# Performance work log

Measured on AMD Instinct MI355X. Metric: run time of the kernel, lower is better.

The kernel has to match this reference:

```python
import jax, jax.numpy as jnp
import numpy as np

S, T, F, J, E, H = 1024, 64, 128, 64, 256, 4
DH = E // H


def layer_norm(x, g, b, eps=1e-10):
    m = jnp.mean(x, axis=-1, keepdims=True)
    v = jnp.mean((x - m) ** 2, axis=-1, keepdims=True)  # population var (correction=0)
    return (x - m) / jnp.sqrt(v + eps) * g + b


def mha(x, Wq, Wk, Wv):
    # x: [B, L, E]; Wq/Wk/Wv: [H, E, DH]. Non-standard: scale AFTER softmax@V.
    q = jnp.einsum('ble,hed->hbld', x, Wq)
    k = jnp.einsum('ble,hed->hbld', x, Wk)
    v = jnp.einsum('ble,hed->hbld', x, Wv)
    w = jax.nn.softmax(jnp.einsum('hbld,hbmd->hblm', q, k), axis=-1)
    o = jnp.einsum('hblm,hbmd->hbld', w, v) / jnp.sqrt(jnp.asarray(Wq.shape[-1], x.dtype))
    h, b, l, d = o.shape
    return jnp.transpose(o, (1, 2, 0, 3)).reshape(b, l, h * d)


def ffn(x, W1, b1, W2, b2):
    return jnp.maximum(x @ W1 + b1, 0.0) @ W2 + b2  # Dropout is identity in eval


def pos_encoding(t, e):
    pos = jnp.arange(t, dtype=jnp.float32)[:, None]
    two_i = jnp.floor(jnp.arange(e, dtype=jnp.float32) / 2.0) * 2.0
    div = jnp.power(jnp.float32(100004.0), two_i / e)
    pe = pos / div  # [t, e]
    pe = pe.at[:, 0::2].set(jnp.sin(pe[:, 0::2]))
    pe = pe.at[:, 1::2].set(jnp.cos(pe[:, 1::2]))
    return pe


def setup_inputs() -> dict:
    key = jax.random.key(0)
    ks = jax.random.split(key, 32)
    s = 0.02
    d = {}
    d['x'] = jax.random.normal(ks[0], (S, T, F + J), dtype=jnp.float32)
    d['gate_W'] = s * jax.random.normal(ks[1], (J, F))
    d['gate_b'] = s * jax.random.normal(ks[2], (F,))
    d['embed_W'] = s * jax.random.normal(ks[3], (F, E))
    d['ln0_g'] = 1.0 + s * jax.random.normal(ks[4], (E,))
    d['ln0_b'] = s * jax.random.normal(ks[5], (E,))
    d['intra_Wq'] = s * jax.random.normal(ks[6], (H, E, DH))
    d['intra_Wk'] = s * jax.random.normal(ks[7], (H, E, DH))
    d['intra_Wv'] = s * jax.random.normal(ks[8], (H, E, DH))
    d['intra_ln_g'] = 1.0 + s * jax.random.normal(ks[9], (E,))
    d['intra_ln_b'] = s * jax.random.normal(ks[10], (E,))
    d['intra_W1'] = s * jax.random.normal(ks[11], (E, 4 * E))
    d['intra_b1'] = s * jax.random.normal(ks[12], (4 * E,))
    d['intra_W2'] = s * jax.random.normal(ks[13], (4 * E, E))
    d['intra_b2'] = s * jax.random.normal(ks[14], (E,))
    d['inter_Wq'] = s * jax.random.normal(ks[15], (H, E, DH))
    d['inter_Wk'] = s * jax.random.normal(ks[16], (H, E, DH))
    d['inter_Wv'] = s * jax.random.normal(ks[17], (H, E, DH))
    d['inter_ln1_g'] = 1.0 + s * jax.random.normal(ks[18], (E,))
    d['inter_ln1_b'] = s * jax.random.normal(ks[19], (E,))
    d['inter_ln2_g'] = 1.0 + s * jax.random.normal(ks[20], (E,))
    d['inter_ln2_b'] = s * jax.random.normal(ks[21], (E,))
    d['inter_W1'] = s * jax.random.normal(ks[22], (E, 4 * E))
    d['inter_b1'] = s * jax.random.normal(ks[23], (4 * E,))
    d['inter_W2'] = s * jax.random.normal(ks[24], (4 * E, E))
    d['inter_b2'] = s * jax.random.normal(ks[25], (E,))
    d['temp_W'] = s * jax.random.normal(ks[26], (E, E))
    d['pred_W'] = s * jax.random.normal(ks[27], (E, 1))
    d['pred_b'] = s * jax.random.normal(ks[28], (1,))
    return d


def reference(x, gate_W, gate_b, embed_W, ln0_g, ln0_b,
              intra_Wq, intra_Wk, intra_Wv, intra_ln_g, intra_ln_b,
              intra_W1, intra_b1, intra_W2, intra_b2,
              inter_Wq, inter_Wk, inter_Wv, inter_ln1_g, inter_ln1_b,
              inter_ln2_g, inter_ln2_b, inter_W1, inter_b1, inter_W2, inter_b2,
              temp_W, pred_W, pred_b):
    # Gating
    x_f = x[..., :F]                       # [S, T, F]
    x_g = x[..., -1, F:]                   # [S, J]
    gate = jax.nn.softmax(x_g @ gate_W + gate_b, axis=-1)[:, None, :]
    x_f = gate * x_f
    # Embed + positional encoding + LN
    emb = x_f @ embed_W                    # [S, T, E]
    res = emb + pos_encoding(T, E)
    ln = layer_norm(res, ln0_g, ln0_b)
    # Intra-stock attention (attend over time axis per stock)
    a = mha(ln, intra_Wq, intra_Wk, intra_Wv)
    r = a + ln
    intra_out = r + ffn(layer_norm(r, intra_ln_g, intra_ln_b), intra_W1, intra_b1, intra_W2, intra_b2)
    # Inter-stock attention (attend over stock axis per timestep)
    xT = jnp.transpose(intra_out, (1, 0, 2))            # [T, S, E]
    xTn = layer_norm(xT, inter_ln1_g, inter_ln1_b)
    a2 = mha(xTn, inter_Wq, inter_Wk, inter_Wv)          # [T, S, E]
    out = jnp.transpose(a2, (1, 0, 2))                   # [S, T, E]
    r2 = out + intra_out
    inter_out = r2 + ffn(layer_norm(r2, inter_ln2_g, inter_ln2_b), inter_W1, inter_b1, inter_W2, inter_b2)
    # Temporal aggregation
    x1 = inter_out @ temp_W                              # [S, T, E]
    cur = x1[..., -1, :][..., :, None]                   # [S, E, 1]
    lam = jax.nn.softmax(jnp.squeeze(x1 @ cur, -1), axis=-1)[:, None, :]  # [S, 1, T]
    agg = jnp.squeeze(lam @ inter_out, -2)               # [S, E]
    # Prediction
    return agg @ pred_W + pred_b                         # [S, 1]
```

## Files before the change

kernel.cpp:

```cpp
#include <hip/hip_runtime.h>


typedef _Float16 h16;
typedef __attribute__((ext_vector_type(8))) _Float16 f16x8;
typedef __attribute__((ext_vector_type(4))) _Float16 f16x4;
typedef __attribute__((ext_vector_type(4))) float f32x4;

__device__ inline float wave_sum(float v){
  #pragma unroll
  for (int o=32;o;o>>=1) v += __shfl_xor(v,o);
  return v;
}
__device__ inline float wave_max(float v){
  #pragma unroll
  for (int o=32;o;o>>=1) v = fmaxf(v,__shfl_xor(v,o));
  return v;
}

__global__ __launch_bounds__(256) void k_pe(float* __restrict__ pe){
  int t = blockIdx.x, i = threadIdx.x;
  float two_i = (float)((i>>1)<<1);
  float dv = powf(100004.0f, two_i*(1.0f/256.0f));
  float v = (float)t / dv;
  pe[t*256+i] = (i&1) ? cosf(v) : sinf(v);
}

__global__ __launch_bounds__(64) void k_gate(const float* __restrict__ x,
    const float* __restrict__ gW, const float* __restrict__ gb,
    float* __restrict__ gate){
  int s = blockIdx.x, lane = threadIdx.x;
  __shared__ float xg[64];
  xg[lane] = x[((size_t)s*64+63)*192 + 128 + lane];
  __syncthreads();
  float a0 = gb[lane], a1 = gb[64+lane];
  #pragma unroll 4
  for (int j=0;j<64;j++){
    float xv = xg[j];
    a0 += xv*gW[j*128+lane];
    a1 += xv*gW[j*128+64+lane];
  }
  float mx = wave_max(fmaxf(a0,a1));
  float e0 = __expf(a0-mx), e1 = __expf(a1-mx);
  float sm = wave_sum(e0+e1);
  gate[s*128+lane]    = e0/sm;
  gate[s*128+64+lane] = e1/sm;
}

__global__ __launch_bounds__(256) void k_t16all(
    const float* __restrict__ q1, const float* __restrict__ k1, const float* __restrict__ v1,
    const float* __restrict__ q2, const float* __restrict__ k2, const float* __restrict__ v2,
    const float* __restrict__ embed_W, const float* __restrict__ temp_W,
    const float* __restrict__ iW1, const float* __restrict__ iW2,
    const float* __restrict__ eW1, const float* __restrict__ eW2,
    h16* __restrict__ base){
  __shared__ float tile[32][33];
  const int b = blockIdx.x, tid = threadIdx.x;
  const float* src; h16* dst; int K, N, tb; bool qkv = false;
  if (b < 384){
    int mat = b>>6; tb = b&63; qkv = true; K = 256; N = 256;
    src = (mat==0)?q1:(mat==1)?k1:(mat==2)?v1:(mat==3)?q2:(mat==4)?k2:v2;
    dst = base + mat*65536;
  } else if (b < 416){ tb = b-384;  K=128;  N=256;  src=embed_W; dst=base+393216; }
  else if (b < 480){ tb = b-416;  K=256;  N=256;  src=temp_W;  dst=base+425984; }
  else if (b < 736){ tb = b-480;  K=256;  N=1024; src=iW1;     dst=base+491520; }
  else if (b < 992){ tb = b-736;  K=1024; N=256;  src=iW2;     dst=base+753664; }
  else if (b < 1248){ tb = b-992; K=256;  N=1024; src=eW1;     dst=base+1015808; }
  else               { tb = b-1248; K=1024; N=256; src=eW2;    dst=base+1277952; }
  const int nt = N>>5;
  const int N0 = (tb & (nt-1))<<5;
  const int K0 = (tb/nt)<<5;
  {
    int r = tid>>3, c0 = (tid&7)<<2;
    int k = K0+r, n = N0+c0;
    const float* p = qkv ? (src + ((n>>6)<<14) + (k<<6) + (n&63))
                         : (src + (size_t)k*N + n);
    float4 v = *(const float4*)p;
    tile[r][c0]=v.x; tile[r][c0+1]=v.y; tile[r][c0+2]=v.z; tile[r][c0+3]=v.w;
  }
  __syncthreads();
  {
    int r = tid>>3, c0 = (tid&7)<<2;
    f16x4 o;
    o[0]=(h16)tile[c0][r]; o[1]=(h16)tile[c0+1][r];
    o[2]=(h16)tile[c0+2][r]; o[3]=(h16)tile[c0+3][r];
    *(f16x4*)(dst + (size_t)(N0+r)*K + K0 + c0) = o;
  }
}

__global__ __launch_bounds__(256) void k_embed(
    const float* __restrict__ x, const h16* __restrict__ Et,
    const float* __restrict__ pe, const float* __restrict__ gate,
    const float* __restrict__ g0, const float* __restrict__ b0,
    float* __restrict__ A){
  __shared__ char pool[65536];
  h16*  As  = (h16*)pool;
  float* res = (float*)pool;
  const int tid = threadIdx.x, lane = tid&63, w = tid>>6;
  const int lr = lane&15, g = lane>>4;
  const int m0 = blockIdx.x<<6;
  #pragma unroll
  for (int it=0; it<8; it++){
    int f4 = it*256 + tid;
    int row = f4>>5, c4 = (f4&31)<<2;
    float4 v = *(const float4*)(x + (size_t)(m0+row)*192 + c4);
    float4 gg = *(const float4*)(gate + (((m0+row)>>6)<<7) + c4);
    v.x*=gg.x; v.y*=gg.y; v.z*=gg.z; v.w*=gg.w;
    int idx = ((row<<7) + c4) ^ ((row&7)<<3);
    f16x4 o; o[0]=(h16)v.x; o[1]=(h16)v.y; o[2]=(h16)v.z; o[3]=(h16)v.w;
    *(f16x4*)&As[idx] = o;
  }
  __syncthreads();
  f32x4 acc[4][4];
  #pragma unroll
  for (int a=0;a<4;a++)
    #pragma unroll
    for (int b=0;b<4;b++) acc[a][b] = (f32x4){0,0,0,0};
  #pragma unroll
  for (int i=0; i<4; i++){
    int kt = (i + w) & 3;
    f16x8 af[4], bf[4];
    #pragma unroll
    for (int rf=0; rf<4; rf++){
      int r = (rf<<4) + lr;
      int idx = ((r<<7) + (kt<<5) + (g<<3)) ^ ((r&7)<<3);
      af[rf] = *(const f16x8*)&As[idx];
    }
    #pragma unroll
    for (int cf=0; cf<4; cf++){
      int n = (w<<6) + (cf<<4) + lr;
      bf[cf] = *(const f16x8*)(Et + (size_t)n*128 + (kt<<5) + (g<<3));
    }
    __builtin_amdgcn_s_setprio(1);
    #pragma unroll
    for (int rf=0; rf<4; rf++)
      #pragma unroll
      for (int cf=0; cf<4; cf++)
        acc[rf][cf] = __builtin_amdgcn_mfma_f32_16x16x32_f16(af[rf], bf[cf], acc[rf][cf], 0,0,0);
    __builtin_amdgcn_s_setprio(0);
  }
  __syncthreads();
  #pragma unroll
  for (int cf=0; cf<4; cf++){
    int col = (w<<6) + (cf<<4) + lr;
    #pragma unroll
    for (int rf=0; rf<4; rf++)
      #pragma unroll
      for (int i=0;i<4;i++){
        int r = (rf<<4) + (g<<2) + i;
        res[(r<<8) + col] = acc[rf][cf][i] + pe[(r<<8) + col];
      }
  }
  __syncthreads();
  {
    float4 gg = *(const float4*)(g0 + (lane<<2));
    float4 bb = *(const float4*)(b0 + (lane<<2));
    for (int rr=0; rr<16; rr++){
      int r = (w<<4) + rr;
      float4 v = *(float4*)&res[(r<<8) + (lane<<2)];
      float sm = wave_sum(v.x+v.y+v.z+v.w);
      float sq = wave_sum(v.x*v.x+v.y*v.y+v.z*v.z+v.w*v.w);
      float mean = sm*(1.f/256.f);
      float rs = rsqrtf(sq*(1.f/256.f) - mean*mean + 1e-10f);
      float4 o;
      o.x=(v.x-mean)*rs*gg.x+bb.x; o.y=(v.y-mean)*rs*gg.y+bb.y;
      o.z=(v.z-mean)*rs*gg.z+bb.z; o.w=(v.w-mean)*rs*gg.w+bb.w;
      *(float4*)(A + (size_t)(m0+r)*256 + (lane<<2)) = o;
    }
  }
}

__global__ __launch_bounds__(512,1) void k_intra(
    const float* __restrict__ A, const h16* __restrict__ Wqkv,
    float* __restrict__ Out){
  __shared__ h16 Xs[64*256];
  __shared__ h16 Qs[4*64*64];
  __shared__ h16 Ks[4*64*64];
  __shared__ h16 VsT[4*64*64];
  __shared__ h16 Ps[8*16*64];
  const int tid = threadIdx.x, lane = tid&63, w = tid>>6;
  const int lr = lane&15, g = lane>>4;
  const int m0 = blockIdx.x<<6;

  #pragma unroll
  for (int rr=0; rr<8; rr++){
    int r = (w<<3) + rr;
    float4 v = *(const float4*)(A + (size_t)(m0+r)*256 + (lane<<2));
    f16x4 o; o[0]=(h16)v.x; o[1]=(h16)v.y; o[2]=(h16)v.z; o[3]=(h16)v.w;
    int idx = ((r<<8) + (lane<<2)) ^ ((r&7)<<3);
    *(f16x4*)&Xs[idx] = o;
  }
  __syncthreads();

  f32x4 acc[4][6];
  #pragma unroll
  for (int a=0;a<4;a++)
    #pragma unroll
    for (int b=0;b<6;b++) acc[a][b] = (f32x4){0,0,0,0};
  #pragma unroll
  for (int kt=0; kt<8; kt++){
    f16x8 af[4], bf[6];
    #pragma unroll
    for (int rf=0; rf<4; rf++){
      int r = (rf<<4) + lr;
      int idx = ((r<<8) + (kt<<5) + (g<<3)) ^ ((r&7)<<3);
      af[rf] = *(const f16x8*)&Xs[idx];
    }
    #pragma unroll
    for (int m=0;m<3;m++)
      #pragma unroll
      for (int cf=0;cf<2;cf++){
        int n = (w<<5) + (cf<<4) + lr;
        bf[m*2+cf] = *(const f16x8*)(Wqkv + (size_t)m*65536 + (size_t)n*256 + (kt<<5) + (g<<3));
      }
    __builtin_amdgcn_s_setprio(1);
    #pragma unroll
    for (int rf=0; rf<4; rf++)
      #pragma unroll
      for (int mc=0; mc<6; mc++)
        acc[rf][mc] = __builtin_amdgcn_mfma_f32_16x16x32_f16(af[rf], bf[mc], acc[rf][mc], 0,0,0);
    __builtin_amdgcn_s_setprio(0);
  }
  #pragma unroll
  for (int cf=0; cf<2; cf++){
    int n = (w<<5) + (cf<<4) + lr;
    int head = n>>6, d = n&63;
    int hb = head<<12;
    int vkey = (d + (d>>3)) & 7;
    #pragma unroll
    for (int rf=0; rf<4; rf++)
      #pragma unroll
      for (int i=0;i<4;i++){
        int qrow = (rf<<4) + (g<<2) + i;
        Qs[hb + (qrow<<6) + (((d>>3) ^ (qrow&7))<<3) + (d&7)] = (h16)acc[rf][0*2+cf][i];
        Ks[hb + (qrow<<6) + (((d>>3) ^ (qrow&7))<<3) + (d&7)] = (h16)acc[rf][1*2+cf][i];
        VsT[hb + (d<<6) + (((qrow>>3) ^ vkey)<<3) + (qrow&7)] = (h16)acc[rf][2*2+cf][i];
      }
  }
  __syncthreads();

  #pragma unroll
  for (int sl=0; sl<2; sl++){
    int slot = w + (sl<<3);
    int head = slot>>2, q0 = (slot&3)<<4;
    const int hb = head<<12;
    f16x8 qf[2];
    #pragma unroll
    for (int ks=0; ks<2; ks++)
      qf[ks] = *(const f16x8*)&Qs[hb + ((q0+lr)<<6) + (((g + (ks<<2)) ^ (lr&7))<<3)];
    f32x4 sa[4];
    #pragma unroll
    for (int mm=0;mm<4;mm++) sa[mm] = (f32x4){0,0,0,0};
    __builtin_amdgcn_s_setprio(1);
    #pragma unroll
    for (int ks=0; ks<2; ks++)
      #pragma unroll
      for (int mm=0;mm<4;mm++){
        int krow = (mm<<4) + lr;
        f16x8 af = *(const f16x8*)&Ks[hb + (krow<<6) + (((g + (ks<<2)) ^ (krow&7))<<3)];
        sa[mm] = __builtin_amdgcn_mfma_f32_16x16x32_f16(af, qf[ks], sa[mm], 0,0,0);
      }
    __builtin_amdgcn_s_setprio(0);
    float pmax = -1e30f;
    #pragma unroll
    for (int mm=0;mm<4;mm++)
      #pragma unroll
      for (int i=0;i<4;i++) pmax = fmaxf(pmax, sa[mm][i]);
    pmax = fmaxf(pmax, __shfl_xor(pmax, 16));
    pmax = fmaxf(pmax, __shfl_xor(pmax, 32));
    float ps = 0.f;
    f16x4 pv[4];
    #pragma unroll
    for (int mm=0;mm<4;mm++)
      #pragma unroll
      for (int i=0;i<4;i++){
        float p = __expf(sa[mm][i] - pmax);
        ps += p;
        pv[mm][i] = (h16)p;
      }
    ps += __shfl_xor(ps, 16);
    ps += __shfl_xor(ps, 32);
    const int pbase = w<<10;
    #pragma unroll
    for (int mm=0;mm<4;mm++){
      int k0 = (mm<<4) + (g<<2);
      int unit = k0>>3, off = k0&7;
      *(f16x4*)&Ps[pbase + (lr<<6) + ((unit ^ (lr&7))<<3) + off] = pv[mm];
    }
    f32x4 oc[4];
    #pragma unroll
    for (int cf=0;cf<4;cf++) oc[cf] = (f32x4){0,0,0,0};
    __builtin_amdgcn_s_setprio(1);
    #pragma unroll
    for (int ks=0; ks<2; ks++){
      f16x8 pa = *(const f16x8*)&Ps[pbase + (lr<<6) + (((g + (ks<<2)) ^ (lr&7))<<3)];
      #pragma unroll
      for (int cf=0;cf<4;cf++){
        int d = (cf<<4) + lr;
        int key = (d + (d>>3)) & 7;
        f16x8 bf = *(const f16x8*)&VsT[hb + (d<<6) + (((g + (ks<<2)) ^ key)<<3)];
        oc[cf] = __builtin_amdgcn_mfma_f32_16x16x32_f16(pa, bf, oc[cf], 0,0,0);
      }
    }
    __builtin_amdgcn_s_setprio(0);
    float linv = 1.0f/(ps*8.0f);
    #pragma unroll
    for (int i=0;i<4;i++){
      float li = __shfl(linv, (g<<4) + (g<<2) + i);
      int row = m0 + q0 + (g<<2) + i;
      #pragma unroll
      for (int cf=0;cf<4;cf++){
        int col = (head<<6) + (cf<<4) + lr;
        size_t ga = (size_t)row*256 + col;
        Out[ga] = oc[cf][i]*li + A[ga];
      }
    }
  }
}

template<bool DOLN>
__global__ __launch_bounds__(512) void k_qkv(
    const float* __restrict__ X,
    const float* __restrict__ lng, const float* __restrict__ lnb,
    const h16* __restrict__ Bt0,
    h16* __restrict__ Qh, h16* __restrict__ Kh, h16* __restrict__ Vh){
  __shared__ h16 Xs[64*256];
  const int tid = threadIdx.x, lane = tid&63, w = tid>>6;
  const int lr = lane&15, g = lane>>4;
  const int m0 = blockIdx.x<<6;
  {
    float4 gg, bb;
    if (DOLN){ gg = *(const float4*)(lng + (lane<<2)); bb = *(const float4*)(lnb + (lane<<2)); }
    #pragma unroll
    for (int rr=0; rr<8; rr++){
      int r = (w<<3) + rr;
      float4 v = *(const float4*)(X + (size_t)(m0+r)*256 + (lane<<2));
      if (DOLN){
        float sm = wave_sum(v.x+v.y+v.z+v.w);
        float sq = wave_sum(v.x*v.x+v.y*v.y+v.z*v.z+v.w*v.w);
        float mean = sm*(1.f/256.f);
        float rs = rsqrtf(sq*(1.f/256.f) - mean*mean + 1e-10f);
        v.x=(v.x-mean)*rs*gg.x+bb.x; v.y=(v.y-mean)*rs*gg.y+bb.y;
        v.z=(v.z-mean)*rs*gg.z+bb.z; v.w=(v.w-mean)*rs*gg.w+bb.w;
      }
      f16x4 o; o[0]=(h16)v.x; o[1]=(h16)v.y; o[2]=(h16)v.z; o[3]=(h16)v.w;
      int idx = ((r<<8) + (lane<<2)) ^ ((r&7)<<3);
      *(f16x4*)&Xs[idx] = o;
    }
  }
  __syncthreads();
  f32x4 acc[4][3];
  #pragma unroll
  for (int a=0;a<4;a++)
    #pragma unroll
    for (int m=0;m<3;m++) acc[a][m] = (f32x4){0,0,0,0};
  #pragma unroll
  for (int i=0; i<8; i++){
    int kt = (i + w) & 7;
    f16x8 af[4], bf[3];
    #pragma unroll
    for (int rf=0; rf<4; rf++){
      int r = (rf<<4) + lr;
      int idx = ((r<<8) + (kt<<5) + (g<<3)) ^ ((r&7)<<3);
      af[rf] = *(const f16x8*)&Xs[idx];
    }
    #pragma unroll
    for (int m=0;m<3;m++){
      int n = (w<<4) + lr;
      bf[m] = *(const f16x8*)(Bt0 + (size_t)m*65536 + (size_t)n*256 + (kt<<5) + (g<<3));
    }
    __builtin_amdgcn_s_setprio(1);
    #pragma unroll
    for (int rf=0; rf<4; rf++)
      #pragma unroll
      for (int m=0;m<3;m++)
        acc[rf][m] = __builtin_amdgcn_mfma_f32_16x16x32_f16(af[rf], bf[m], acc[rf][m], 0,0,0);
    __builtin_amdgcn_s_setprio(0);
  }
  const int col = (w<<4) + lr;
  #pragma unroll
  for (int m=0;m<3;m++){
    h16* dst = (m==0)?Qh:(m==1)?Kh:Vh;
    #pragma unroll
    for (int rf=0; rf<4; rf++)
      #pragma unroll
      for (int i=0;i<4;i++){
        int r = m0 + (rf<<4) + (g<<2) + i;
        dst[(size_t)r*128 + col] = (h16)acc[rf][m][i];
      }
  }
}

template<int NT, int QG>
__global__ __launch_bounds__(256) void k_attn16(
    const h16* __restrict__ Qh, const h16* __restrict__ Kh, const h16* __restrict__ Vh,
    const float* __restrict__ Resid, float* __restrict__ Out, int hbase){
  __shared__ h16 Ks[64*64];
  __shared__ h16 VsT[64*64];
  __shared__ h16 Ps[4*QG*16*64];
  const int tid = threadIdx.x, lane = tid&63, w = tid>>6;
  const int lr = lane&15, g = lane>>4;
  int hh, t=0, qc=0, s=0;
  if (NT==1){ s = blockIdx.x; hh = blockIdx.y; }
  else      { hh = blockIdx.x; t = blockIdx.y; qc = blockIdx.z; }
  const int ccol = hh<<6;
  const int gcol = (hbase+hh)<<6;

  f16x8 qf[QG][2];
  #pragma unroll
  for (int grp=0; grp<QG; grp++){
    int ql = grp*64 + (w<<4) + lr;
    size_t m = (NT==1) ? ((size_t)s*64 + ql) : (((size_t)qc*(64*QG) + ql)*64 + t);
    const h16* qp = Qh + m*128 + ccol + (g<<3);
    qf[grp][0] = *(const f16x8*)qp;
    qf[grp][1] = *(const f16x8*)(qp + 32);
  }

  f32x4 oc[QG][4];
  float m_r[QG], l_r[QG];
  #pragma unroll
  for (int grp=0; grp<QG; grp++){
    #pragma unroll
    for (int cf=0;cf<4;cf++) oc[grp][cf] = (f32x4){0,0,0,0};
    m_r[grp] = -1e30f; l_r[grp] = 0.f;
  }

  for (int kb=0; kb<NT; kb++){
    __syncthreads();
    #pragma unroll
    for (int it=0; it<2; it++){
      int u = it*256 + tid;
      int row = u>>3, un = u&7;
      size_t m = (NT==1) ? ((size_t)s*64 + row) : (((size_t)kb*64 + row)*64 + t);
      f16x8 kv = *(const f16x8*)(Kh + m*128 + ccol + (un<<3));
      *(f16x8*)&Ks[(row<<6) + ((un ^ (row&7))<<3)] = kv;
      f16x8 vv = *(const f16x8*)(Vh + m*128 + ccol + (un<<3));
      #pragma unroll
      for (int j=0;j<8;j++){
        int d = (un<<3) + j;
        int key = (d + un) & 7;
        VsT[(d<<6) + ((((row>>3) ^ key))<<3) + (row&7)] = vv[j];
      }
    }
    __syncthreads();
    #pragma unroll
    for (int grp=0; grp<QG; grp++){
      f32x4 sa[4];
      #pragma unroll
      for (int mm=0;mm<4;mm++) sa[mm] = (f32x4){0,0,0,0};
      __builtin_amdgcn_s_setprio(1);
      #pragma unroll
      for (int ks=0; ks<2; ks++){
        #pragma unroll
        for (int mm=0;mm<4;mm++){
          int krow = (mm<<4) + lr;
          f16x8 af = *(const f16x8*)&Ks[(krow<<6) + (((g + (ks<<2)) ^ (krow&7))<<3)];
          sa[mm] = __builtin_amdgcn_mfma_f32_16x16x32_f16(af, qf[grp][ks], sa[mm], 0,0,0);
        }
      }
      __builtin_amdgcn_s_setprio(0);
      float pmax = -1e30f;
      #pragma unroll
      for (int mm=0;mm<4;mm++)
        #pragma unroll
        for (int i=0;i<4;i++) pmax = fmaxf(pmax, sa[mm][i]);
      pmax = fmaxf(pmax, __shfl_xor(pmax, 16));
      pmax = fmaxf(pmax, __shfl_xor(pmax, 32));
      float mn = fmaxf(m_r[grp], pmax);
      float sca = __expf(m_r[grp] - mn);
      m_r[grp] = mn;
      float ps = 0.f;
      f16x4 pv[4];
      #pragma unroll
      for (int mm=0;mm<4;mm++){
        #pragma unroll
        for (int i=0;i<4;i++){
          float p = __expf(sa[mm][i] - mn);
          ps += p;
          pv[mm][i] = (h16)p;
        }
      }
      ps += __shfl_xor(ps, 16);
      ps += __shfl_xor(ps, 32);
      l_r[grp] = l_r[grp]*sca + ps;
      const int pbase = ((w*QG + grp)<<10);
      #pragma unroll
      for (int mm=0;mm<4;mm++){
        int k0 = (mm<<4) + (g<<2);
        int unit = k0>>3, off = k0&7;
        *(f16x4*)&Ps[pbase + (lr<<6) + ((unit ^ (lr&7))<<3) + off] = pv[mm];
      }
      #pragma unroll
      for (int i=0;i<4;i++){
        float si = __shfl(sca, (g<<4) + (g<<2) + i);
        #pragma unroll
        for (int cf=0;cf<4;cf++) oc[grp][cf][i] *= si;
      }
      __builtin_amdgcn_s_setprio(1);
      #pragma unroll
      for (int ks=0; ks<2; ks++){
        f16x8 pa = *(const f16x8*)&Ps[pbase + (lr<<6) + (((g + (ks<<2)) ^ (lr&7))<<3)];
        #pragma unroll
        for (int cf=0;cf<4;cf++){
          int d = (cf<<4) + lr;
          int key = (d + (d>>3)) & 7;
          f16x8 bf = *(const f16x8*)&VsT[(d<<6) + (((g + (ks<<2)) ^ key)<<3)];
          oc[grp][cf] = __builtin_amdgcn_mfma_f32_16x16x32_f16(pa, bf, oc[grp][cf], 0,0,0);
        }
      }
      __builtin_amdgcn_s_setprio(0);
    }
  }
  #pragma unroll
  for (int grp=0; grp<QG; grp++){
    float linv = 1.0f/(l_r[grp]*8.0f);
    #pragma unroll
    for (int i=0;i<4;i++){
      float li = __shfl(linv, (g<<4) + (g<<2) + i);
      int ql = grp*64 + (w<<4) + (g<<2) + i;
      size_t m = (NT==1) ? ((size_t)s*64 + ql) : (((size_t)qc*(64*QG) + ql)*64 + t);
      #pragma unroll
      for (int cf=0;cf<4;cf++){
        int d = (cf<<4) + lr;
        size_t ga = m*256 + gcol + d;
        Out[ga] = oc[grp][cf][i]*li + Resid[ga];
      }
    }
  }
}

__global__ __launch_bounds__(512,1) void k_ffn5(
    const float* X, float* Out,
    const float* __restrict__ lng, const float* __restrict__ lnb,
    const h16* __restrict__ W1t, const float* __restrict__ b1,
    const h16* __restrict__ W2t, const float* __restrict__ b2){
  __shared__ h16 Xs[64*256];
  __shared__ h16 Hc[64*1024];
  const int tid  = threadIdx.x;
  const int lane = tid & 63;
  const int w    = tid >> 6;
  const int r0   = blockIdx.x << 6;
  const int lr   = lane & 15;
  const int g    = lane >> 4;
  {
    float4 gg = *(const float4*)(lng + (lane<<2));
    float4 bb = *(const float4*)(lnb + (lane<<2));
    #pragma unroll
    for (int rr=0; rr<8; rr++){
      int r = (w<<3) + rr;
      float4 v = *(const float4*)(X + (size_t)(r0+r)*256 + (lane<<2));
      float sm = wave_sum(v.x+v.y+v.z+v.w);
      float sq = wave_sum(v.x*v.x+v.y*v.y+v.z*v.z+v.w*v.w);
      float mean = sm*(1.f/256.f);
      float rs = rsqrtf(sq*(1.f/256.f) - mean*mean + 1e-10f);
      f16x4 o;
      o[0]=(h16)((v.x-mean)*rs*gg.x+bb.x); o[1]=(h16)((v.y-mean)*rs*gg.y+bb.y);
      o[2]=(h16)((v.z-mean)*rs*gg.z+bb.z); o[3]=(h16)((v.w-mean)*rs*gg.w+bb.w);
      int idx = ((r<<8) + (lane<<2)) ^ ((r&7)<<3);
      *(f16x4*)&Xs[idx] = o;
    }
  }
  __syncthreads();
  {
    f32x4 acc1[4][8];
    #pragma unroll
    for (int a=0;a<4;a++)
      #pragma unroll
      for (int b=0;b<8;b++) acc1[a][b] = (f32x4){0,0,0,0};
    #pragma unroll
    for (int i=0; i<8; i++){
      int kt = (i + w) & 7;
      f16x8 af[4], bf[8];
      #pragma unroll
      for (int rf=0; rf<4; rf++){
        int r = (rf<<4) + lr;
        int idx = ((r<<8) + (kt<<5) + (g<<3)) ^ ((r&7)<<3);
        af[rf] = *(const f16x8*)&Xs[idx];
      }
      #pragma unroll
      for (int cf=0; cf<8; cf++){
        int n = (w<<7) + (cf<<4) + lr;
        bf[cf] = *(const f16x8*)(W1t + (size_t)n*256 + (kt<<5) + (g<<3));
      }
      __builtin_amdgcn_s_setprio(1);
      #pragma unroll
      for (int rf=0; rf<4; rf++)
        #pragma unroll
        for (int cf=0; cf<8; cf++)
          acc1[rf][cf] = __builtin_amdgcn_mfma_f32_16x16x32_f16(
              af[rf], bf[cf], acc1[rf][cf], 0, 0, 0);
      __builtin_amdgcn_s_setprio(0);
    }
    #pragma unroll
    for (int cf=0; cf<8; cf++){
      int cl = (w<<7) + (cf<<4) + lr;
      float bv = b1[cl];
      #pragma unroll
      for (int rf=0; rf<4; rf++){
        #pragma unroll
        for (int i=0;i<4;i++){
          int r = (rf<<4) + (g<<2) + i;
          float hv = fmaxf(acc1[rf][cf][i] + bv, 0.f);
          int idx = ((r<<10) + cl) ^ ((r&7)<<3);
          Hc[idx] = (h16)hv;
        }
      }
    }
  }
  __syncthreads();
  f32x4 acc2[4][2];
  #pragma unroll
  for (int a=0;a<4;a++){ acc2[a][0]=(f32x4){0,0,0,0}; acc2[a][1]=(f32x4){0,0,0,0}; }
  #pragma unroll 4
  for (int i=0; i<32; i++){
    int kt = (i + (w<<2)) & 31;
    f16x8 af[4], bf[2];
    #pragma unroll
    for (int rf=0; rf<4; rf++){
      int r = (rf<<4) + lr;
      int idx = ((r<<10) + (kt<<5) + (g<<3)) ^ ((r&7)<<3);
      af[rf] = *(const f16x8*)&Hc[idx];
    }
    #pragma unroll
    for (int cf=0; cf<2; cf++){
      int n = (w<<5) + (cf<<4) + lr;
      bf[cf] = *(const f16x8*)(W2t + (size_t)n*1024 + (kt<<5) + (g<<3));
    }
    __builtin_amdgcn_s_setprio(1);
    #pragma unroll
    for (int rf=0; rf<4; rf++)
      #pragma unroll
      for (int cf=0; cf<2; cf++)
        acc2[rf][cf] = __builtin_amdgcn_mfma_f32_16x16x32_f16(
            af[rf], bf[cf], acc2[rf][cf], 0, 0, 0);
    __builtin_amdgcn_s_setprio(0);
  }
  #pragma unroll
  for (int cf=0; cf<2; cf++){
    int col = (w<<5) + (cf<<4) + lr;
    float bv = b2[col];
    #pragma unroll
    for (int rf=0; rf<4; rf++){
      #pragma unroll
      for (int i=0;i<4;i++){
        size_t r = (size_t)r0 + (rf<<4) + (g<<2) + i;
        float res = X[r*256 + col];
        Out[r*256 + col] = acc2[rf][cf][i] + bv + res;
      }
    }
  }
}

__global__ __launch_bounds__(256) void k_head(
    const float* __restrict__ Bb, const h16* __restrict__ Tt,
    const float* __restrict__ predW, const float* __restrict__ predb,
    float* __restrict__ out){
  __shared__ h16 Xs[64*256];
  __shared__ float X1s[64*256];
  __shared__ float lam[64];
  __shared__ float red[4];
  const int tid = threadIdx.x, lane = tid&63, w = tid>>6;
  const int lr = lane&15, g = lane>>4;
  const size_t m0 = (size_t)blockIdx.x<<6;
  #pragma unroll
  for (int it=0; it<16; it++){
    int f4 = it*256 + tid;
    int row = f4>>6, c4 = (f4&63)<<2;
    float4 v = *(const float4*)(Bb + (m0+row)*256 + c4);
    int idx = ((row<<8) + c4) ^ ((row&7)<<3);
    f16x4 o; o[0]=(h16)v.x; o[1]=(h16)v.y; o[2]=(h16)v.z; o[3]=(h16)v.w;
    *(f16x4*)&Xs[idx] = o;
  }
  __syncthreads();
  f32x4 acc[4][4];
  #pragma unroll
  for (int rf=0;rf<4;rf++)
    #pragma unroll
    for (int cf=0;cf<4;cf++) acc[rf][cf] = (f32x4){0,0,0,0};
  #pragma unroll
  for (int kt=0; kt<8; kt++){
    f16x8 af[4], bf[4];
    #pragma unroll
    for (int rf=0; rf<4; rf++){
      int r = (rf<<4) + lr;
      int idx = ((r<<8) + (kt<<5) + (g<<3)) ^ ((r&7)<<3);
      af[rf] = *(const f16x8*)&Xs[idx];
    }
    #pragma unroll
    for (int cf=0; cf<4; cf++){
      int n = (w<<6) + (cf<<4) + lr;
      bf[cf] = *(const f16x8*)(Tt + (size_t)n*256 + (kt<<5) + (g<<3));
    }
    __builtin_amdgcn_s_setprio(1);
    #pragma unroll
    for (int rf=0; rf<4; rf++)
      #pragma unroll
      for (int cf=0; cf<4; cf++)
        acc[rf][cf] = __builtin_amdgcn_mfma_f32_16x16x32_f16(af[rf], bf[cf], acc[rf][cf], 0,0,0);
    __builtin_amdgcn_s_setprio(0);
  }
  #pragma unroll
  for (int cf=0; cf<4; cf++){
    int col = (w<<6) + (cf<<4) + lr;
    #pragma unroll
    for (int rf=0; rf<4; rf++)
      #pragma unroll
      for (int i=0;i<4;i++){
        int r = (rf<<4) + (g<<2) + i;
        X1s[(r<<8) + col] = acc[rf][cf][i];
      }
  }
  __syncthreads();
  float lg[16];
  for (int r=0;r<16;r++){
    int trow = (w<<4) + r;
    float4 xa = *(float4*)&X1s[(trow<<8) + (lane<<2)];
    float4 xc = *(float4*)&X1s[(63<<8) + (lane<<2)];
    lg[r] = wave_sum(xa.x*xc.x + xa.y*xc.y + xa.z*xc.z + xa.w*xc.w);
  }
  if (lane==0){
    #pragma unroll
    for (int r=0;r<16;r++) lam[(w<<4)+r] = lg[r];
  }
  __syncthreads();
  if (tid < 64){
    float v = lam[tid];
    float mx = wave_max(v);
    float p = __expf(v-mx);
    float sm = wave_sum(p);
    lam[tid] = p/sm;
  }
  __syncthreads();
  float ag = 0.f;
  for (int t=0;t<64;t++)
    ag += lam[t]*(float)Xs[((t<<8)+tid) ^ ((t&7)<<3)];
  float wsum = wave_sum(ag * predW[tid]);
  if (lane==0) red[w] = wsum;
  __syncthreads();
  if (tid==0) out[blockIdx.x] = red[0]+red[1]+red[2]+red[3] + predb[0];
}

extern "C" void kernel_launch(void* const* d_in, const int* in_sizes, int n_in,
                              void* d_out, int out_size, void* d_ws, size_t ws_size,
                              hipStream_t stream){
  const float* x       = (const float*)d_in[0];
  const float* gate_W  = (const float*)d_in[1];
  const float* gate_b  = (const float*)d_in[2];
  const float* embed_W = (const float*)d_in[3];
  const float* ln0_g   = (const float*)d_in[4];
  const float* ln0_b   = (const float*)d_in[5];
  const float* iln_g   = (const float*)d_in[9];
  const float* iln_b   = (const float*)d_in[10];
  const float* iW1     = (const float*)d_in[11];
  const float* ib1     = (const float*)d_in[12];
  const float* iW2     = (const float*)d_in[13];
  const float* ib2     = (const float*)d_in[14];
  const float* eln1_g  = (const float*)d_in[18];
  const float* eln1_b  = (const float*)d_in[19];
  const float* eln2_g  = (const float*)d_in[20];
  const float* eln2_b  = (const float*)d_in[21];
  const float* eW1     = (const float*)d_in[22];
  const float* eb1     = (const float*)d_in[23];
  const float* eW2     = (const float*)d_in[24];
  const float* eb2     = (const float*)d_in[25];
  const float* temp_W  = (const float*)d_in[26];
  const float* pred_W  = (const float*)d_in[27];
  const float* pred_b  = (const float*)d_in[28];
  float* out = (float*)d_out;

  float* pe    = (float*)d_ws;
  float* gate  = pe + 16384;
  h16* fQKV = (h16*)((char*)d_ws + ((size_t)4<<20));
  h16* fE   = fQKV + 393216;
  h16* fT   = fE + 32768;
  h16* fW1i = fT + 65536;
  h16* fW2i = fW1i + 262144;
  h16* fW1e = fW2i + 262144;
  h16* fW2e = fW1e + 262144;
  const size_t MR = (size_t)65536*256, MH = (size_t)65536*128;
  float* A  = (float*)((char*)d_ws + ((size_t)8<<20));
  float* Bb = A + MR;
  h16* Qh = (h16*)(Bb + MR);
  h16* Kh = Qh + MH;
  h16* Vh = Kh + MH;

  k_pe  <<<64,  256, 0, stream>>>(pe);
  k_gate<<<1024, 64, 0, stream>>>(x, gate_W, gate_b, gate);
  k_t16all<<<1504,256,0,stream>>>(
      (const float*)d_in[6],(const float*)d_in[7],(const float*)d_in[8],
      (const float*)d_in[15],(const float*)d_in[16],(const float*)d_in[17],
      embed_W, temp_W, iW1, iW2, eW1, eW2, fQKV);

  k_embed<<<1024,256,0,stream>>>(x, fE, pe, gate, ln0_g, ln0_b, A);

  k_intra<<<1024,512,0,stream>>>(A, fQKV, Bb);
  k_ffn5<<<1024,512,0,stream>>>(Bb, Bb, iln_g, iln_b, fW1i, ib1, fW2i, ib2);

  for (int hp=0; hp<2; hp++){
    int hb = hp*2;
    k_qkv<true><<<1024,512,0,stream>>>(Bb, eln1_g, eln1_b,
        fQKV + 3*65536 + hb*16384, Qh, Kh, Vh);
    k_attn16<16,1><<<dim3(2,64,16),256,0,stream>>>(Qh, Kh, Vh, Bb, Bb, hb);
  }
  k_ffn5<<<1024,512,0,stream>>>(Bb, Bb, eln2_g, eln2_b, fW1e, eb1, fW2e, eb2);

  k_head<<<1024,256,0,stream>>>(Bb, fT, pred_W, pred_b, out);
}
```

Baseline: 722.9 us.

## Split FFN layernorm into separate kernel and restructure FFN with LDS-staged weight chunks

```diff
diff --git a/kernel.cpp b/kernel.cpp
--- a/kernel.cpp
+++ b/kernel.cpp
@@ -180,7 +180,6 @@
   const int tid = threadIdx.x, lane = tid&63, w = tid>>6;
   const int lr = lane&15, g = lane>>4;
   const int m0 = blockIdx.x<<6;
-
   #pragma unroll
   for (int rr=0; rr<8; rr++){
     int r = (w<<3) + rr;
@@ -190,7 +189,6 @@
     *(f16x4*)&Xs[idx] = o;
   }
   __syncthreads();
-
   f32x4 acc[4][6];
   #pragma unroll
   for (int a=0;a<4;a++)
@@ -237,7 +235,6 @@
       }
   }
   __syncthreads();
-
   #pragma unroll
   for (int sl=0; sl<2; sl++){
     int slot = w + (sl<<3);
@@ -528,126 +525,147 @@
   }
 }
 
-__global__ __launch_bounds__(512,1) void k_ffn5(
-    const float* X, float* Out,
-    const float* __restrict__ lng, const float* __restrict__ lnb,
+__global__ __launch_bounds__(256) void k_lnh(const float* __restrict__ in,
+    const float* __restrict__ g, const float* __restrict__ b,
+    h16* __restrict__ out){
+  const int wv = threadIdx.x>>6, lane = threadIdx.x&63;
+  const size_t row = (size_t)blockIdx.x*4 + wv;
+  float4 v = *(const float4*)(in + row*256 + (lane<<2));
+  float sm = wave_sum(v.x+v.y+v.z+v.w);
+  float sq = wave_sum(v.x*v.x+v.y*v.y+v.z*v.z+v.w*v.w);
+  float mean = sm*(1.f/256.f);
+  float rs = rsqrtf(sq*(1.f/256.f) - mean*mean + 1e-10f);
+  float4 gg = *(const float4*)(g + (lane<<2));
+  float4 bb = *(const float4*)(b + (lane<<2));
+  f16x4 o;
+  o[0]=(h16)((v.x-mean)*rs*gg.x+bb.x); o[1]=(h16)((v.y-mean)*rs*gg.y+bb.y);
+  o[2]=(h16)((v.z-mean)*rs*gg.z+bb.z); o[3]=(h16)((v.w-mean)*rs*gg.w+bb.w);
+  *(f16x4*)(out + row*256 + (lane<<2)) = o;
+}
+
+__global__ __launch_bounds__(512,1) void k_ffn7(
+    const h16* __restrict__ Xh, const float* __restrict__ Resid,
+    float* __restrict__ Out,
     const h16* __restrict__ W1t, const float* __restrict__ b1,
     const h16* __restrict__ W2t, const float* __restrict__ b2){
-  __shared__ h16 Xs[64*256];
-  __shared__ h16 Hc[64*1024];
-  const int tid  = threadIdx.x;
-  const int lane = tid & 63;
-  const int w    = tid >> 6;
-  const int r0   = blockIdx.x << 6;
-  const int lr   = lane & 15;
-  const int g    = lane >> 4;
-  {
-    float4 gg = *(const float4*)(lng + (lane<<2));
-    float4 bb = *(const float4*)(lnb + (lane<<2));
-    #pragma unroll
-    for (int rr=0; rr<8; rr++){
-      int r = (w<<3) + rr;
-      float4 v = *(const float4*)(X + (size_t)(r0+r)*256 + (lane<<2));
-      float sm = wave_sum(v.x+v.y+v.z+v.w);
-      float sq = wave_sum(v.x*v.x+v.y*v.y+v.z*v.z+v.w*v.w);
-      float mean = sm*(1.f/256.f);
-      float rs = rsqrtf(sq*(1.f/256.f) - mean*mean + 1e-10f);
-      f16x4 o;
-      o[0]=(h16)((v.x-mean)*rs*gg.x+bb.x); o[1]=(h16)((v.y-mean)*rs*gg.y+bb.y);
-      o[2]=(h16)((v.z-mean)*rs*gg.z+bb.z); o[3]=(h16)((v.w-mean)*rs*gg.w+bb.w);
-      int idx = ((r<<8) + (lane<<2)) ^ ((r&7)<<3);
-      *(f16x4*)&Xs[idx] = o;
-    }
-  }
-  __syncthreads();
-  {
-    f32x4 acc1[4][8];
-    #pragma unroll
-    for (int a=0;a<4;a++)
-      #pragma unroll
-      for (int b=0;b<8;b++) acc1[a][b] = (f32x4){0,0,0,0};
-    #pragma unroll
-    for (int i=0; i<8; i++){
-      int kt = (i + w) & 7;
-      f16x8 af[4], bf[8];
-      #pragma unroll
-      for (int rf=0; rf<4; rf++){
-        int r = (rf<<4) + lr;
-        int idx = ((r<<8) + (kt<<5) + (g<<3)) ^ ((r&7)<<3);
-        af[rf] = *(const f16x8*)&Xs[idx];
-      }
-      #pragma unroll
-      for (int cf=0; cf<8; cf++){
-        int n = (w<<7) + (cf<<4) + lr;
-        bf[cf] = *(const f16x8*)(W1t + (size_t)n*256 + (kt<<5) + (g<<3));
-      }
-      __builtin_amdgcn_s_setprio(1);
+  __shared__ h16 W1c[128*256];
+  __shared__ h16 W2c[256*128];
+  __shared__ h16 Pool[64*256];
+  const int tid = threadIdx.x, lane = tid&63, w = tid>>6;
+  const int lr = lane&15, g = lane>>4;
+  const size_t R0 = (size_t)blockIdx.x<<8;
+
+  float b2v[2];
+  b2v[0] = b2[(w<<5)+lr]; b2v[1] = b2[(w<<5)+16+lr];
+
+  f32x4 acc2[4][4][2];
+  #pragma unroll
+  for (int rt=0;rt<4;rt++)
+    #pragma unroll
+    for (int rf=0;rf<4;rf++){
+      acc2[rt][rf][0]=(f32x4){0,0,0,0}; acc2[rt][rf][1]=(f32x4){0,0,0,0};
+    }
+
+  for (int hc=0; hc<8; hc++){
+    __syncthreads();
+    {
+      int n1 = tid>>2, p1 = tid&3;
+      const h16* s1 = W1t + (size_t)((hc<<7) + n1)*256;
+      #pragma unroll
+      for (int j=0;j<8;j++){
+        int u = (p1<<3)+j;
+        *(f16x8*)&W1c[(n1<<8) + ((u ^ (n1&7))<<3)] = *(const f16x8*)(s1 + (u<<3));
+      }
+      int n2 = tid>>1, p2 = tid&1;
+      const h16* s2 = W2t + (size_t)n2*1024 + (hc<<7);
+      #pragma unroll
+      for (int j=0;j<8;j++){
+        int u = (p2<<3)+j;
+        *(f16x8*)&W2c[(n2<<7) + ((u ^ (n2&7))<<3)] = *(const f16x8*)(s2 + (u<<3));
+      }
+    }
+    float b1v = b1[(hc<<7) + (w<<4) + lr];
+
+    #pragma unroll
+    for (int rt=0; rt<4; rt++){
+      __syncthreads();
+      {
+        const h16* xsrc = Xh + (R0 + (rt<<6))*256;
+        #pragma unroll
+        for (int it=0; it<4; it++){
+          int e = it*512 + tid;
+          int row = e>>5, u = e&31;
+          *(f16x8*)&Pool[(row<<8) + ((u ^ (row&7))<<3)] =
+              *(const f16x8*)(xsrc + (row<<8) + (u<<3));
+        }
+      }
+      __syncthreads();
+      f32x4 acc1[4];
+      #pragma unroll
+      for (int rf=0;rf<4;rf++) acc1[rf] = (f32x4){0,0,0,0};
+      const int n1 = (w<<4) + lr;
+      #pragma unroll
+      for (int kt=0; kt<8; kt++){
+        f16x8 af[4];
+        #pragma unroll
+        for (int rf=0; rf<4; rf++){
+          int r = (rf<<4) + lr;
+          af[rf] = *(const f16x8*)&Pool[((r<<8) + (kt<<5) + (g<<3)) ^ ((r&7)<<3)];
+        }
+        f16x8 bf = *(const f16x8*)&W1c[(n1<<8) + ((((kt<<2)+g) ^ (n1&7))<<3)];
+        __builtin_amdgcn_s_setprio(1);
+        #pragma unroll
+        for (int rf=0; rf<4; rf++)
+          acc1[rf] = __builtin_amdgcn_mfma_f32_16x16x32_f16(af[rf], bf, acc1[rf], 0,0,0);
+        __builtin_amdgcn_s_setprio(0);
+      }
+      __syncthreads();
       #pragma unroll
       for (int rf=0; rf<4; rf++)
-        #pragma unroll
-        for (int cf=0; cf<8; cf++)
-          acc1[rf][cf] = __builtin_amdgcn_mfma_f32_16x16x32_f16(
-              af[rf], bf[cf], acc1[rf][cf], 0, 0, 0);
-      __builtin_amdgcn_s_setprio(0);
-    }
-    #pragma unroll
-    for (int cf=0; cf<8; cf++){
-      int cl = (w<<7) + (cf<<4) + lr;
-      float bv = b1[cl];
-      #pragma unroll
-      for (int rf=0; rf<4; rf++){
         #pragma unroll
         for (int i=0;i<4;i++){
           int r = (rf<<4) + (g<<2) + i;
-          float hv = fmaxf(acc1[rf][cf][i] + bv, 0.f);
-          int idx = ((r<<10) + cl) ^ ((r&7)<<3);
-          Hc[idx] = (h16)hv;
+          float hv = fmaxf(acc1[rf][i] + b1v, 0.f);
+          Pool[((r<<7) + n1) ^ ((r&7)<<3)] = (h16)hv;
         }
-      }
-    }
-  }
-  __syncthreads();
-  f32x4 acc2[4][2];
-  #pragma unroll
-  for (int a=0;a<4;a++){ acc2[a][0]=(f32x4){0,0,0,0}; acc2[a][1]=(f32x4){0,0,0,0}; }
-  #pragma unroll 4
-  for (int i=0; i<32; i++){
-    int kt = (i + (w<<2)) & 31;
-    f16x8 af[4], bf[2];
-    #pragma unroll
-    for (int rf=0; rf<4; rf++){
-      int r = (rf<<4) + lr;
-      int idx = ((r<<10) + (kt<<5) + (g<<3)) ^ ((r&7)<<3);
-      af[rf] = *(const f16x8*)&Hc[idx];
-    }
+      __syncthreads();
+      #pragma unroll
+      for (int kt=0; kt<4; kt++){
+        f16x8 af[4], bf[2];
+        #pragma unroll
+        for (int rf=0; rf<4; rf++){
+          int r = (rf<<4) + lr;
+          af[rf] = *(const f16x8*)&Pool[((r<<7) + (kt<<5) + (g<<3)) ^ ((r&7)<<3)];
+        }
+        #pragma unroll
+        for (int cf=0; cf<2; cf++){
+          int n = (w<<5) + (cf<<4) + lr;
+          bf[cf] = *(const f16x8*)&W2c[(n<<7) + ((((kt<<2)+g) ^ (n&7))<<3)];
+        }
+        __builtin_amdgcn_s_setprio(1);
+        #pragma unroll
+        for (int rf=0; rf<4; rf++)
+          #pragma unroll
+          for (int cf=0; cf<2; cf++)
+            acc2[rt][rf][cf] = __builtin_amdgcn_mfma_f32_16x16x32_f16(
+                af[rf], bf[cf], acc2[rt][rf][cf], 0,0,0);
+        __builtin_amdgcn_s_setprio(0);
+      }
+    }
+  }
+  #pragma unroll
+  for (int rt=0; rt<4; rt++)
     #pragma unroll
     for (int cf=0; cf<2; cf++){
-      int n = (w<<5) + (cf<<4) + lr;
-      bf[cf] = *(const f16x8*)(W2t + (size_t)n*1024 + (kt<<5) + (g<<3));
-    }
-    __builtin_amdgcn_s_setprio(1);
-    #pragma unroll
-    for (int rf=0; rf<4; rf++)
-      #pragma unroll
-      for (int cf=0; cf<2; cf++)
-        acc2[rf][cf] = __builtin_amdgcn_mfma_f32_16x16x32_f16(
-            af[rf], bf[cf], acc2[rf][cf], 0, 0, 0);
-    __builtin_amdgcn_s_setprio(0);
-  }
-  #pragma unroll
-  for (int cf=0; cf<2; cf++){
-    int col = (w<<5) + (cf<<4) + lr;
-    float bv = b2[col];
-    #pragma unroll
-    for (int rf=0; rf<4; rf++){
-      #pragma unroll
-      for (int i=0;i<4;i++){
-        size_t r = (size_t)r0 + (rf<<4) + (g<<2) + i;
-        float res = X[r*256 + col];
-        Out[r*256 + col] = acc2[rf][cf][i] + bv + res;
-      }
-    }
-  }
+      int col = (w<<5) + (cf<<4) + lr;
+      #pragma unroll
+      for (int rf=0; rf<4; rf++)
+        #pragma unroll
+        for (int i=0;i<4;i++){
+          size_t r = R0 + (rt<<6) + (rf<<4) + (g<<2) + i;
+          Out[r*256 + col] = acc2[rt][rf][cf][i] + b2v[cf] + Resid[r*256 + col];
+        }
+    }
 }
 
 __global__ __launch_bounds__(256) void k_head(
@@ -782,6 +800,7 @@
   h16* Qh = (h16*)(Bb + MR);
   h16* Kh = Qh + MH;
   h16* Vh = Kh + MH;
+  h16* Xh = (h16*)A;
 
   k_pe  <<<64,  256, 0, stream>>>(pe);
   k_gate<<<1024, 64, 0, stream>>>(x, gate_W, gate_b, gate);
@@ -793,7 +812,8 @@
   k_embed<<<1024,256,0,stream>>>(x, fE, pe, gate, ln0_g, ln0_b, A);
 
   k_intra<<<1024,512,0,stream>>>(A, fQKV, Bb);
-  k_ffn5<<<1024,512,0,stream>>>(Bb, Bb, iln_g, iln_b, fW1i, ib1, fW2i, ib2);
+  k_lnh<<<16384,256,0,stream>>>(Bb, iln_g, iln_b, Xh);
+  k_ffn7<<<256,512,0,stream>>>(Xh, Bb, Bb, fW1i, ib1, fW2i, ib2);
 
   for (int hp=0; hp<2; hp++){
     int hb = hp*2;
@@ -801,7 +821,8 @@
         fQKV + 3*65536 + hb*16384, Qh, Kh, Vh);
     k_attn16<16,1><<<dim3(2,64,16),256,0,stream>>>(Qh, Kh, Vh, Bb, Bb, hb);
   }
-  k_ffn5<<<1024,512,0,stream>>>(Bb, Bb, eln2_g, eln2_b, fW1e, eb1, fW2e, eb2);
+  k_lnh<<<16384,256,0,stream>>>(Bb, eln2_g, eln2_b, Xh);
+  k_ffn7<<<256,512,0,stream>>>(Xh, Bb, Bb, fW1e, eb1, fW2e, eb2);
 
   k_head<<<1024,256,0,stream>>>(Bb, fT, pred_W, pred_b, out);
 }
```

New measurement: 868.9 us. 1.2x slower.
